# Kernel tuning notes

Measured on AMD Instinct MI355X. Metric: run time of the kernel, lower is better.

The kernel has to match this reference:

```python
import jax, jax.numpy as jnp
import numpy as np

H = 4096          # hidden_size
I = 2048          # moe_intermediate_size * n_shared_experts
SWIGLU_LIMIT = 10.0
QMAX = 127.0


def _quantize_weight(w):
    # per-output-channel symmetric int8 quantization of a float weight [out, in]
    s = jnp.maximum(jnp.max(jnp.abs(w), axis=1) / QMAX, 1e-8)      # [out]
    q = jnp.clip(jnp.round(w / s[:, None]), -QMAX, QMAX)           # int8-valued
    return q.astype(jnp.float32), s.astype(jnp.float32)


def setup_inputs() -> dict:
    key = jax.random.key(0)
    ks = jax.random.split(key, 4)
    x = jax.random.normal(ks[0], (2, 4096, H), dtype=jnp.float32)
    w_gate, s_wgate = _quantize_weight(jax.random.normal(ks[1], (I, H)) * 0.02)
    w_up, s_wup = _quantize_weight(jax.random.normal(ks[2], (I, H)) * 0.02)
    w_down, s_wdown = _quantize_weight(jax.random.normal(ks[3], (H, I)) * 0.02)
    inv_gate = jnp.ones((H,), jnp.float32)
    inv_up = jnp.ones((H,), jnp.float32)
    inv_inter = jnp.ones((I,), jnp.float32)
    return {"x": x, "w_gate": w_gate, "s_wgate": s_wgate, "w_up": w_up,
            "s_wup": s_wup, "w_down": w_down, "s_wdown": s_wdown,
            "inv_gate": inv_gate, "inv_up": inv_up, "inv_inter": inv_inter}


def _dynamic_quant(x, inv_smooth):
    # per-token symmetric int8 dynamic quant with smoothing scale
    xs = x.astype(jnp.float32) * inv_smooth                        # [T, D]
    scale = jnp.maximum(jnp.max(jnp.abs(xs), axis=-1, keepdims=True) / QMAX, 1e-8)
    q = jnp.clip(jnp.round(xs / scale), -QMAX, QMAX)
    return q, scale


def _quant_gemm(q, x_scale, w_q, w_scale):
    acc = q @ w_q.T                                                # fp32 accumulate
    return acc * x_scale * w_scale[None, :]


def reference(x, w_gate, s_wgate, w_up, s_wup, w_down, s_wdown,
              inv_gate, inv_up, inv_inter):
    orig_shape = x.shape
    x_flat = x.reshape(-1, H).astype(jnp.bfloat16)                 # [T, H]
    qg, sg = _dynamic_quant(x_flat, inv_gate)
    qu, su = _dynamic_quant(x_flat, inv_up)
    gate_out = _quant_gemm(qg, sg, w_gate, s_wgate)                # [T, I]
    up_out = _quant_gemm(qu, su, w_up, s_wup)                      # [T, I]
    inter = jax.nn.silu(gate_out) * up_out
    inter = jnp.clip(inter, -SWIGLU_LIMIT, SWIGLU_LIMIT).astype(jnp.bfloat16)
    qi, si = _dynamic_quant(inter, inv_inter)
    out = _quant_gemm(qi, si, w_down, s_wdown)                     # [T, H]
    return out.reshape(orig_shape)
```

## Files before the change

kernel.cpp:

```cpp
#include <hip/hip_runtime.h>
#include <hip/hip_bf16.h>


typedef __attribute__((ext_vector_type(4))) int i32x4;

__device__ __forceinline__ void async16(void* lds, const void* g) {
  __builtin_amdgcn_global_load_lds(
      (const __attribute__((address_space(1))) void*)g,
      (__attribute__((address_space(3))) void*)lds, 16, 0, 0);
}

__device__ __forceinline__ i32x4 mfma_i8(i32x4 a, i32x4 b, i32x4 c) {
  return __builtin_amdgcn_mfma_i32_16x16x64_i8(a, b, c, 0, 0, 0);
}

__device__ __forceinline__ float bf16_rne_f(float f) {
  unsigned u = __float_as_uint(f);
  u += 0x7fffu + ((u >> 16) & 1u);
  return __uint_as_float(u & 0xffff0000u);
}

__device__ __forceinline__ unsigned short bf16_bits(float f) {
  unsigned u = __float_as_uint(f);
  u += 0x7fffu + ((u >> 16) & 1u);
  return (unsigned short)(u >> 16);
}

__device__ __forceinline__ float bf16_to_f(unsigned short h) {
  return __uint_as_float(((unsigned)h) << 16);
}

#define BARRIER __builtin_amdgcn_s_barrier()
#define WAIT_VM6 asm volatile("s_waitcnt vmcnt(6) lgkmcnt(0)" ::: "memory")
#define WAIT_VM4 asm volatile("s_waitcnt vmcnt(4) lgkmcnt(0)" ::: "memory")
#define WAIT_VM0 asm volatile("s_waitcnt vmcnt(0) lgkmcnt(0)" ::: "memory")

__global__ void wconv_kernel(const float* __restrict__ w,
                             signed char* __restrict__ wq, int n) {
  int i = (blockIdx.x * 256 + threadIdx.x) * 4;
  if (i >= n) return;
  float4 f = *(const float4*)(w + i);
  signed char c[4] __attribute__((aligned(4)));
  c[0] = (signed char)(int)rintf(f.x);
  c[1] = (signed char)(int)rintf(f.y);
  c[2] = (signed char)(int)rintf(f.z);
  c[3] = (signed char)(int)rintf(f.w);
  *(int*)(wq + i) = *(const int*)c;
}

__global__ __launch_bounds__(256) void quant_x_kernel(
    const float* __restrict__ x, const float* __restrict__ invg,
    const float* __restrict__ invu, signed char* __restrict__ qg,
    signed char* __restrict__ qu, float* __restrict__ sg,
    float* __restrict__ su, int H) {
  const int t = blockIdx.x, tid = threadIdx.x;
  const float* xr = x + (size_t)t * H;
  const int c0 = tid * 16;
  float xg[16], xu[16];
  float mg = 0.f, mu = 0.f;
#pragma unroll
  for (int v = 0; v < 4; ++v) {
    float4 f = *(const float4*)(xr + c0 + v * 4);
    float4 ig = *(const float4*)(invg + c0 + v * 4);
    float4 iu = *(const float4*)(invu + c0 + v * 4);
    float b0 = bf16_rne_f(f.x), b1 = bf16_rne_f(f.y);
    float b2 = bf16_rne_f(f.z), b3 = bf16_rne_f(f.w);
    xg[v * 4 + 0] = b0 * ig.x; xg[v * 4 + 1] = b1 * ig.y;
    xg[v * 4 + 2] = b2 * ig.z; xg[v * 4 + 3] = b3 * ig.w;
    xu[v * 4 + 0] = b0 * iu.x; xu[v * 4 + 1] = b1 * iu.y;
    xu[v * 4 + 2] = b2 * iu.z; xu[v * 4 + 3] = b3 * iu.w;
#pragma unroll
    for (int j = 0; j < 4; ++j) {
      mg = fmaxf(mg, fabsf(xg[v * 4 + j]));
      mu = fmaxf(mu, fabsf(xu[v * 4 + j]));
    }
  }
#pragma unroll
  for (int off = 32; off > 0; off >>= 1) {
    mg = fmaxf(mg, __shfl_xor(mg, off));
    mu = fmaxf(mu, __shfl_xor(mu, off));
  }
  __shared__ float smg[4], smu[4];
  if ((tid & 63) == 0) { smg[tid >> 6] = mg; smu[tid >> 6] = mu; }
  __syncthreads();
  mg = fmaxf(fmaxf(smg[0], smg[1]), fmaxf(smg[2], smg[3]));
  mu = fmaxf(fmaxf(smu[0], smu[1]), fmaxf(smu[2], smu[3]));
  const float scg = fmaxf(mg / 127.0f, 1e-8f);
  const float scu = fmaxf(mu / 127.0f, 1e-8f);
  signed char og[16] __attribute__((aligned(16)));
  signed char ou[16] __attribute__((aligned(16)));
#pragma unroll
  for (int j = 0; j < 16; ++j) {
    og[j] = (signed char)(int)fminf(fmaxf(rintf(xg[j] / scg), -127.f), 127.f);
    ou[j] = (signed char)(int)fminf(fmaxf(rintf(xu[j] / scu), -127.f), 127.f);
  }
  *(i32x4*)(qg + (size_t)t * H + c0) = *(const i32x4*)og;
  *(i32x4*)(qu + (size_t)t * H + c0) = *(const i32x4*)ou;
  if (tid == 0) { sg[t] = scg; su[t] = scu; }
}

#define G1_STAGE(b, kk)                                                       \
  {                                                                           \
    _Pragma("unroll") for (int p = 0; p < 2; ++p) {                           \
      const int g = p * 512 + tid;                                            \
      const int r = g >> 2;                                                   \
      const int c = (g & 3) ^ ((r >> 1) & 3);                                 \
      const size_t so = (size_t)r * H + (kk) + c * 16;                        \
      async16(&Ag[b][g * 16], qg + rowbase_a + so);                           \
      async16(&Au[b][g * 16], qu + rowbase_a + so);                           \
    }                                                                         \
    {                                                                         \
      const int r2 = tid >> 2;                                                \
      const int c2 = (tid & 3) ^ ((r2 >> 1) & 3);                             \
      const size_t so2 = (size_t)r2 * H + (kk) + c2 * 16;                     \
      async16(&Bg[b][tid * 16], wg + rowbase_b + so2);                        \
      async16(&Bu[b][tid * 16], wu + rowbase_b + so2);                        \
    }                                                                         \
  }

__global__ __launch_bounds__(512, 2) void gemm1_kernel(
    const signed char* __restrict__ qg, const signed char* __restrict__ qu,
    const float* __restrict__ sg, const float* __restrict__ su,
    const signed char* __restrict__ wg, const signed char* __restrict__ wu,
    const float* __restrict__ swg, const float* __restrict__ swu,
    unsigned short* __restrict__ inter, int H, int I) {
  __shared__ signed char Ag[3][256 * 64] __attribute__((aligned(16)));
  __shared__ signed char Au[3][256 * 64] __attribute__((aligned(16)));
  __shared__ signed char Bg[3][128 * 64] __attribute__((aligned(16)));
  __shared__ signed char Bu[3][128 * 64] __attribute__((aligned(16)));
  const int tid = threadIdx.x;
  const int lane = tid & 63, wave = tid >> 6;
  const int row0 = blockIdx.x * 256, col0 = blockIdx.y * 128;
  const int wm = wave >> 1, wn = wave & 1;
  const int mrow = lane & 15, quad = lane >> 4;
  const int NT = H >> 6;
  const size_t rowbase_a = (size_t)row0 * H;
  const size_t rowbase_b = (size_t)col0 * H;

  int offA[4], offB[4];
#pragma unroll
  for (int i = 0; i < 4; ++i) {
    const int ra = wm * 64 + i * 16 + mrow;
    offA[i] = ra * 64 + ((quad ^ ((ra >> 1) & 3)) << 4);
    const int rb = wn * 64 + i * 16 + mrow;
    offB[i] = rb * 64 + ((quad ^ ((rb >> 1) & 3)) << 4);
  }

  i32x4 accG[4][4], accU[4][4];
#pragma unroll
  for (int i = 0; i < 4; ++i)
#pragma unroll
    for (int j = 0; j < 4; ++j) {
      accG[i][j] = i32x4{0, 0, 0, 0};
      accU[i][j] = i32x4{0, 0, 0, 0};
    }

  G1_STAGE(0, 0);
  G1_STAGE(1, 64);
  asm volatile("s_waitcnt vmcnt(6)" ::: "memory");
  BARRIER;

  int bc = 0, bs = 2;
  for (int kt = 0; kt < NT; ++kt) {
    if (kt + 2 < NT) G1_STAGE(bs, (kt + 2) << 6);

    i32x4 aG[4], aU[4], bG[4], bU[4];
#pragma unroll
    for (int i = 0; i < 4; ++i) {
      aG[i] = *(const i32x4*)(&Ag[bc][0] + offA[i]);
      aU[i] = *(const i32x4*)(&Au[bc][0] + offA[i]);
      bG[i] = *(const i32x4*)(&Bg[bc][0] + offB[i]);
      bU[i] = *(const i32x4*)(&Bu[bc][0] + offB[i]);
    }
    __builtin_amdgcn_s_setprio(1);
#pragma unroll
    for (int i = 0; i < 4; ++i)
#pragma unroll
      for (int j = 0; j < 4; ++j) {
        accG[i][j] = mfma_i8(aG[i], bG[j], accG[i][j]);
        accU[i][j] = mfma_i8(aU[i], bU[j], accU[i][j]);
      }
    __builtin_amdgcn_s_setprio(0);

    if (kt + 2 < NT) {
      WAIT_VM6;
      BARRIER;
    } else if (kt + 1 < NT) {
      WAIT_VM0;
      BARRIER;
    }
    bc = (bc == 2) ? 0 : bc + 1;
    bs = (bs == 2) ? 0 : bs + 1;
  }

  float swgc[4], swuc[4];
#pragma unroll
  for (int j = 0; j < 4; ++j) {
    const int c = col0 + wn * 64 + j * 16 + mrow;
    swgc[j] = swg[c];
    swuc[j] = swu[c];
  }
#pragma unroll
  for (int i = 0; i < 4; ++i) {
#pragma unroll
    for (int r = 0; r < 4; ++r) {
      const int row = row0 + wm * 64 + i * 16 + quad * 4 + r;
      const float sgr = sg[row], sur = su[row];
#pragma unroll
      for (int j = 0; j < 4; ++j) {
        const int c = col0 + wn * 64 + j * 16 + mrow;
        const float g = (float)accG[i][j][r] * sgr * swgc[j];
        const float u = (float)accU[i][j][r] * sur * swuc[j];
        const float sig = 1.f / (1.f + expf(-g));
        float v = (g * sig) * u;
        v = fminf(fmaxf(v, -10.f), 10.f);
        inter[(size_t)row * I + c] = bf16_bits(v);
      }
    }
  }
}

__global__ __launch_bounds__(256) void quant_i_kernel(
    const unsigned short* __restrict__ inter, const float* __restrict__ invi,
    signed char* __restrict__ qi, float* __restrict__ si, int I) {
  const int t = blockIdx.x, tid = threadIdx.x;
  const unsigned short* ir = inter + (size_t)t * I;
  const int c0 = tid * 8;
  uint4 pk = *(const uint4*)(ir + c0);
  float4 i0 = *(const float4*)(invi + c0);
  float4 i1 = *(const float4*)(invi + c0 + 4);
  float xs[8];
  xs[0] = bf16_to_f(pk.x & 0xffffu) * i0.x;
  xs[1] = bf16_to_f(pk.x >> 16) * i0.y;
  xs[2] = bf16_to_f(pk.y & 0xffffu) * i0.z;
  xs[3] = bf16_to_f(pk.y >> 16) * i0.w;
  xs[4] = bf16_to_f(pk.z & 0xffffu) * i1.x;
  xs[5] = bf16_to_f(pk.z >> 16) * i1.y;
  xs[6] = bf16_to_f(pk.w & 0xffffu) * i1.z;
  xs[7] = bf16_to_f(pk.w >> 16) * i1.w;
  float m = 0.f;
#pragma unroll
  for (int j = 0; j < 8; ++j) m = fmaxf(m, fabsf(xs[j]));
#pragma unroll
  for (int off = 32; off > 0; off >>= 1) m = fmaxf(m, __shfl_xor(m, off));
  __shared__ float sm[4];
  if ((tid & 63) == 0) sm[tid >> 6] = m;
  __syncthreads();
  m = fmaxf(fmaxf(sm[0], sm[1]), fmaxf(sm[2], sm[3]));
  const float s = fmaxf(m / 127.0f, 1e-8f);
  signed char o[8] __attribute__((aligned(8)));
#pragma unroll
  for (int j = 0; j < 8; ++j)
    o[j] = (signed char)(int)fminf(fmaxf(rintf(xs[j] / s), -127.f), 127.f);
  *(unsigned long long*)(qi + (size_t)t * I + c0) = *(const unsigned long long*)o;
  if (tid == 0) si[t] = s;
}

#define G2_STAGE(b, kk)                                                       \
  {                                                                           \
    _Pragma("unroll") for (int p = 0; p < 2; ++p) {                           \
      const int g = p * 512 + tid;                                            \
      const int r = g >> 2;                                                   \
      const int c = (g & 3) ^ ((r >> 1) & 3);                                 \
      const size_t so = (size_t)r * I + (kk) + c * 16;                        \
      async16(&As[b][g * 16], qi + rowbase_a + so);                           \
      async16(&Bs[b][g * 16], wd + rowbase_b + so);                           \
    }                                                                         \
  }

__global__ __launch_bounds__(512, 2) void gemm2_kernel(
    const signed char* __restrict__ qi, const float* __restrict__ si,
    const signed char* __restrict__ wd, const float* __restrict__ swd,
    float* __restrict__ out, int H, int I) {
  __shared__ signed char As[3][256 * 64] __attribute__((aligned(16)));
  __shared__ signed char Bs[3][256 * 64] __attribute__((aligned(16)));
  const int tid = threadIdx.x;
  const int lane = tid & 63, wave = tid >> 6;
  const int row0 = blockIdx.x * 256, col0 = blockIdx.y * 256;
  const int wm = wave >> 2, wn = wave & 3;
  const int mrow = lane & 15, quad = lane >> 4;
  const int NT = I >> 6;
  const size_t rowbase_a = (size_t)row0 * I;
  const size_t rowbase_b = (size_t)col0 * I;

  int offA[8], offB[4];
#pragma unroll
  for (int i = 0; i < 8; ++i) {
    const int ra = wm * 128 + i * 16 + mrow;
    offA[i] = ra * 64 + ((quad ^ ((ra >> 1) & 3)) << 4);
  }
#pragma unroll
  for (int j = 0; j < 4; ++j) {
    const int rb = wn * 64 + j * 16 + mrow;
    offB[j] = rb * 64 + ((quad ^ ((rb >> 1) & 3)) << 4);
  }

  i32x4 acc[8][4];
#pragma unroll
  for (int i = 0; i < 8; ++i)
#pragma unroll
    for (int j = 0; j < 4; ++j) acc[i][j] = i32x4{0, 0, 0, 0};

  G2_STAGE(0, 0);
  G2_STAGE(1, 64);
  asm volatile("s_waitcnt vmcnt(4)" ::: "memory");
  BARRIER;

  int bc = 0, bs = 2;
  for (int kt = 0; kt < NT; ++kt) {
    if (kt + 2 < NT) G2_STAGE(bs, (kt + 2) << 6);

    i32x4 a[8], b[4];
#pragma unroll
    for (int i = 0; i < 8; ++i) a[i] = *(const i32x4*)(&As[bc][0] + offA[i]);
#pragma unroll
    for (int j = 0; j < 4; ++j) b[j] = *(const i32x4*)(&Bs[bc][0] + offB[j]);

    __builtin_amdgcn_s_setprio(1);
#pragma unroll
    for (int i = 0; i < 8; ++i)
#pragma unroll
      for (int j = 0; j < 4; ++j) acc[i][j] = mfma_i8(a[i], b[j], acc[i][j]);
    __builtin_amdgcn_s_setprio(0);

    if (kt + 2 < NT) {
      WAIT_VM4;
      BARRIER;
    } else if (kt + 1 < NT) {
      WAIT_VM0;
      BARRIER;
    }
    bc = (bc == 2) ? 0 : bc + 1;
    bs = (bs == 2) ? 0 : bs + 1;
  }

  float swc[4];
#pragma unroll
  for (int j = 0; j < 4; ++j) swc[j] = swd[col0 + wn * 64 + j * 16 + mrow];
#pragma unroll
  for (int i = 0; i < 8; ++i) {
#pragma unroll
    for (int r = 0; r < 4; ++r) {
      const int row = row0 + wm * 128 + i * 16 + quad * 4 + r;
      const float sir = si[row];
#pragma unroll
      for (int j = 0; j < 4; ++j) {
        const int c = col0 + wn * 64 + j * 16 + mrow;
        out[(size_t)row * H + c] = (float)acc[i][j][r] * sir * swc[j];
      }
    }
  }
}

extern "C" void kernel_launch(void* const* d_in, const int* in_sizes, int n_in,
                              void* d_out, int out_size, void* d_ws,
                              size_t ws_size, hipStream_t stream) {
  const float* x = (const float*)d_in[0];
  const float* w_gate = (const float*)d_in[1];
  const float* s_wgate = (const float*)d_in[2];
  const float* w_up = (const float*)d_in[3];
  const float* s_wup = (const float*)d_in[4];
  const float* w_down = (const float*)d_in[5];
  const float* s_wdown = (const float*)d_in[6];
  const float* inv_gate = (const float*)d_in[7];
  const float* inv_up = (const float*)d_in[8];
  const float* inv_inter = (const float*)d_in[9];
  float* out = (float*)d_out;

  const int H = in_sizes[6];
  const int I = in_sizes[2];
  const int T = in_sizes[0] / H;

  char* ws = (char*)d_ws;
  size_t off = 0;
  signed char* wqg = (signed char*)(ws + off); off += (size_t)I * H;
  signed char* wqu = (signed char*)(ws + off); off += (size_t)I * H;
  signed char* wqd = (signed char*)(ws + off); off += (size_t)H * I;
  signed char* qg  = (signed char*)(ws + off); off += (size_t)T * H;
  signed char* qu  = (signed char*)(ws + off); off += (size_t)T * H;
  unsigned short* inter = (unsigned short*)(ws + off); off += (size_t)T * I * 2;
  float* sg = (float*)(ws + off); off += (size_t)T * 4;
  float* su = (float*)(ws + off); off += (size_t)T * 4;
  float* si = (float*)(ws + off); off += (size_t)T * 4;
  signed char* qi = qg;

  const int nW = I * H;
  wconv_kernel<<<nW / 1024, 256, 0, stream>>>(w_gate, wqg, nW);
  wconv_kernel<<<nW / 1024, 256, 0, stream>>>(w_up, wqu, nW);
  wconv_kernel<<<nW / 1024, 256, 0, stream>>>(w_down, wqd, nW);

  quant_x_kernel<<<T, 256, 0, stream>>>(x, inv_gate, inv_up, qg, qu, sg, su, H);

  dim3 g1(T / 256, I / 128);
  gemm1_kernel<<<g1, 512, 0, stream>>>(qg, qu, sg, su, wqg, wqu, s_wgate,
                                       s_wup, inter, H, I);

  quant_i_kernel<<<T, 256, 0, stream>>>(inter, inv_inter, qi, si, I);

  dim3 g2(T / 256, H / 256);
  gemm2_kernel<<<g2, 512, 0, stream>>>(qi, si, wqd, s_wdown, out, H, I);
}
```

Baseline: 648.1 us.

## Split GEMM main loops into barrier-synchronized half-phases and deepen gemm2 pipeline

```diff
diff --git a/kernel.cpp b/kernel.cpp
--- a/kernel.cpp
+++ b/kernel.cpp
@@ -31,9 +31,11 @@
 }
 
 #define BARRIER __builtin_amdgcn_s_barrier()
-#define WAIT_VM6 asm volatile("s_waitcnt vmcnt(6) lgkmcnt(0)" ::: "memory")
-#define WAIT_VM4 asm volatile("s_waitcnt vmcnt(4) lgkmcnt(0)" ::: "memory")
-#define WAIT_VM0 asm volatile("s_waitcnt vmcnt(0) lgkmcnt(0)" ::: "memory")
+#define LGKM0 asm volatile("s_waitcnt lgkmcnt(0)" ::: "memory")
+#define WAIT_VM8 asm volatile("s_waitcnt vmcnt(8)" ::: "memory")
+#define WAIT_VM6 asm volatile("s_waitcnt vmcnt(6)" ::: "memory")
+#define WAIT_VM4 asm volatile("s_waitcnt vmcnt(4)" ::: "memory")
+#define WAIT_VM0 asm volatile("s_waitcnt vmcnt(0)" ::: "memory")
 
 __global__ void wconv_kernel(const float* __restrict__ w,
                              signed char* __restrict__ wq, int n) {
@@ -99,22 +101,37 @@
   if (tid == 0) { sg[t] = scg; su[t] = scu; }
 }
 
-#define G1_STAGE(b, kk)                                                       \
+#define G1_STAGE_G(b, kt)                                                     \
   {                                                                           \
     _Pragma("unroll") for (int p = 0; p < 2; ++p) {                           \
-      const int g = p * 512 + tid;                                            \
-      const int r = g >> 2;                                                   \
-      const int c = (g & 3) ^ ((r >> 1) & 3);                                 \
-      const size_t so = (size_t)r * H + (kk) + c * 16;                        \
-      async16(&Ag[b][g * 16], qg + rowbase_a + so);                           \
-      async16(&Au[b][g * 16], qu + rowbase_a + so);                           \
+      const int g_ = p * 512 + tid;                                           \
+      const int r_ = g_ >> 2;                                                 \
+      const int c_ = (g_ & 3) ^ ((r_ >> 1) & 3);                              \
+      async16(&Ag[b][g_ * 16],                                                \
+              qg + rowbase_a + (size_t)r_ * H + ((kt) << 6) + c_ * 16);       \
     }                                                                         \
     {                                                                         \
-      const int r2 = tid >> 2;                                                \
-      const int c2 = (tid & 3) ^ ((r2 >> 1) & 3);                             \
-      const size_t so2 = (size_t)r2 * H + (kk) + c2 * 16;                     \
-      async16(&Bg[b][tid * 16], wg + rowbase_b + so2);                        \
-      async16(&Bu[b][tid * 16], wu + rowbase_b + so2);                        \
+      const int r_ = tid >> 2;                                                \
+      const int c_ = (tid & 3) ^ ((r_ >> 1) & 3);                             \
+      async16(&Bg[b][tid * 16],                                               \
+              wg + rowbase_b + (size_t)r_ * H + ((kt) << 6) + c_ * 16);       \
+    }                                                                         \
+  }
+
+#define G1_STAGE_U(b, kt)                                                     \
+  {                                                                           \
+    _Pragma("unroll") for (int p = 0; p < 2; ++p) {                           \
+      const int g_ = p * 512 + tid;                                           \
+      const int r_ = g_ >> 2;                                                 \
+      const int c_ = (g_ & 3) ^ ((r_ >> 1) & 3);                              \
+      async16(&Au[b][g_ * 16],                                                \
+              qu + rowbase_a + (size_t)r_ * H + ((kt) << 6) + c_ * 16);       \
+    }                                                                         \
+    {                                                                         \
+      const int r_ = tid >> 2;                                                \
+      const int c_ = (tid & 3) ^ ((r_ >> 1) & 3);                             \
+      async16(&Bu[b][tid * 16],                                               \
+              wu + rowbase_b + (size_t)r_ * H + ((kt) << 6) + c_ * 16);       \
     }                                                                         \
   }
 
@@ -155,31 +172,48 @@
       accU[i][j] = i32x4{0, 0, 0, 0};
     }
 
-  G1_STAGE(0, 0);
-  G1_STAGE(1, 64);
-  asm volatile("s_waitcnt vmcnt(6)" ::: "memory");
+  G1_STAGE_G(0, 0);
+  G1_STAGE_U(0, 0);
+  G1_STAGE_G(1, 1);
+  G1_STAGE_U(1, 1);
+  WAIT_VM6;
   BARRIER;
 
-  int bc = 0, bs = 2;
+  int bc = 0;
   for (int kt = 0; kt < NT; ++kt) {
-    if (kt + 2 < NT) G1_STAGE(bs, (kt + 2) << 6);
-
-    i32x4 aG[4], aU[4], bG[4], bU[4];
+    const int bs = (bc >= 1) ? bc - 1 : 2;
+
+    if (kt + 2 < NT) G1_STAGE_G(bs, kt + 2);
+    i32x4 aG[4], bG[4];
 #pragma unroll
     for (int i = 0; i < 4; ++i) {
       aG[i] = *(const i32x4*)(&Ag[bc][0] + offA[i]);
+      bG[i] = *(const i32x4*)(&Bg[bc][0] + offB[i]);
+    }
+    BARRIER;
+    LGKM0;
+    __builtin_amdgcn_s_setprio(1);
+#pragma unroll
+    for (int i = 0; i < 4; ++i)
+#pragma unroll
+      for (int j = 0; j < 4; ++j) accG[i][j] = mfma_i8(aG[i], bG[j], accG[i][j]);
+    __builtin_amdgcn_s_setprio(0);
+    BARRIER;
+
+    if (kt + 2 < NT) G1_STAGE_U(bs, kt + 2);
+    i32x4 aU[4], bU[4];
+#pragma unroll
+    for (int i = 0; i < 4; ++i) {
       aU[i] = *(const i32x4*)(&Au[bc][0] + offA[i]);
-      bG[i] = *(const i32x4*)(&Bg[bc][0] + offB[i]);
       bU[i] = *(const i32x4*)(&Bu[bc][0] + offB[i]);
     }
+    BARRIER;
+    LGKM0;
     __builtin_amdgcn_s_setprio(1);
 #pragma unroll
     for (int i = 0; i < 4; ++i)
 #pragma unroll
-      for (int j = 0; j < 4; ++j) {
-        accG[i][j] = mfma_i8(aG[i], bG[j], accG[i][j]);
-        accU[i][j] = mfma_i8(aU[i], bU[j], accU[i][j]);
-      }
+      for (int j = 0; j < 4; ++j) accU[i][j] = mfma_i8(aU[i], bU[j], accU[i][j]);
     __builtin_amdgcn_s_setprio(0);
 
     if (kt + 2 < NT) {
@@ -189,8 +223,7 @@
       WAIT_VM0;
       BARRIER;
     }
-    bc = (bc == 2) ? 0 : bc + 1;
-    bs = (bs == 2) ? 0 : bs + 1;
+    bc = (bc >= 2) ? 0 : bc + 1;
   }
 
   float swgc[4], swuc[4];
@@ -256,15 +289,25 @@
   if (tid == 0) si[t] = s;
 }
 
-#define G2_STAGE(b, kk)                                                       \
+#define G2_STAGE_A(b, kt)                                                     \
   {                                                                           \
     _Pragma("unroll") for (int p = 0; p < 2; ++p) {                           \
-      const int g = p * 512 + tid;                                            \
-      const int r = g >> 2;                                                   \
-      const int c = (g & 3) ^ ((r >> 1) & 3);                                 \
-      const size_t so = (size_t)r * I + (kk) + c * 16;                        \
-      async16(&As[b][g * 16], qi + rowbase_a + so);                           \
-      async16(&Bs[b][g * 16], wd + rowbase_b + so);                           \
+      const int g_ = p * 512 + tid;                                           \
+      const int r_ = g_ >> 2;                                                 \
+      const int c_ = (g_ & 3) ^ ((r_ >> 1) & 3);                              \
+      async16(&As[b][g_ * 16],                                                \
+              qi + rowbase_a + (size_t)r_ * I + ((kt) << 6) + c_ * 16);       \
+    }                                                                         \
+  }
+
+#define G2_STAGE_B(b, kt)                                                     \
+  {                                                                           \
+    _Pragma("unroll") for (int p = 0; p < 2; ++p) {                           \
+      const int g_ = p * 512 + tid;                                           \
+      const int r_ = g_ >> 2;                                                 \
+      const int c_ = (g_ & 3) ^ ((r_ >> 1) & 3);                              \
+      async16(&Bs[b][g_ * 16],                                                \
+              wd + rowbase_b + (size_t)r_ * I + ((kt) << 6) + c_ * 16);       \
     }                                                                         \
   }
 
@@ -272,8 +315,8 @@
     const signed char* __restrict__ qi, const float* __restrict__ si,
     const signed char* __restrict__ wd, const float* __restrict__ swd,
     float* __restrict__ out, int H, int I) {
-  __shared__ signed char As[3][256 * 64] __attribute__((aligned(16)));
-  __shared__ signed char Bs[3][256 * 64] __attribute__((aligned(16)));
+  __shared__ signed char As[4][256 * 64] __attribute__((aligned(16)));
+  __shared__ signed char Bs[4][256 * 64] __attribute__((aligned(16)));
   const int tid = threadIdx.x;
   const int lane = tid & 63, wave = tid >> 6;
   const int row0 = blockIdx.x * 256, col0 = blockIdx.y * 256;
@@ -301,37 +344,61 @@
 #pragma unroll
     for (int j = 0; j < 4; ++j) acc[i][j] = i32x4{0, 0, 0, 0};
 
-  G2_STAGE(0, 0);
-  G2_STAGE(1, 64);
-  asm volatile("s_waitcnt vmcnt(4)" ::: "memory");
+  G2_STAGE_A(0, 0);
+  G2_STAGE_B(0, 0);
+  G2_STAGE_A(1, 1);
+  G2_STAGE_B(1, 1);
+  G2_STAGE_A(2, 2);
+  G2_STAGE_B(2, 2);
+  WAIT_VM8;
   BARRIER;
 
-  int bc = 0, bs = 2;
+  int bc = 0;
   for (int kt = 0; kt < NT; ++kt) {
-    if (kt + 2 < NT) G2_STAGE(bs, (kt + 2) << 6);
-
-    i32x4 a[8], b[4];
-#pragma unroll
-    for (int i = 0; i < 8; ++i) a[i] = *(const i32x4*)(&As[bc][0] + offA[i]);
+    const int bs = (kt + 3) & 3;
+
+    if (kt + 3 < NT) G2_STAGE_A(bs, kt + 3);
+    i32x4 a[4], b[4];
 #pragma unroll
     for (int j = 0; j < 4; ++j) b[j] = *(const i32x4*)(&Bs[bc][0] + offB[j]);
-
+#pragma unroll
+    for (int i = 0; i < 4; ++i) a[i] = *(const i32x4*)(&As[bc][0] + offA[i]);
+    BARRIER;
+    LGKM0;
     __builtin_amdgcn_s_setprio(1);
 #pragma unroll
-    for (int i = 0; i < 8; ++i)
+    for (int i = 0; i < 4; ++i)
 #pragma unroll
       for (int j = 0; j < 4; ++j) acc[i][j] = mfma_i8(a[i], b[j], acc[i][j]);
     __builtin_amdgcn_s_setprio(0);
-
-    if (kt + 2 < NT) {
+    BARRIER;
+
+    if (kt + 3 < NT) G2_STAGE_B(bs, kt + 3);
+    i32x4 a2[4];
+#pragma unroll
+    for (int i = 0; i < 4; ++i)
+      a2[i] = *(const i32x4*)(&As[bc][0] + offA[4 + i]);
+    BARRIER;
+    LGKM0;
+    __builtin_amdgcn_s_setprio(1);
+#pragma unroll
+    for (int i = 0; i < 4; ++i)
+#pragma unroll
+      for (int j = 0; j < 4; ++j)
+        acc[4 + i][j] = mfma_i8(a2[i], b[j], acc[4 + i][j]);
+    __builtin_amdgcn_s_setprio(0);
+
+    if (kt + 3 < NT) {
+      WAIT_VM8;
+      BARRIER;
+    } else if (kt + 2 < NT) {
       WAIT_VM4;
       BARRIER;
     } else if (kt + 1 < NT) {
       WAIT_VM0;
       BARRIER;
     }
-    bc = (bc == 2) ? 0 : bc + 1;
-    bs = (bs == 2) ? 0 : bs + 1;
+    bc = (bc + 1) & 3;
   }
 
   float swc[4];
```

Result: slower. 670.1 us (+3.4%).
